# Kernel tuning notes

Measured on AMD Instinct MI355X. Metric: run time of the kernel, lower is better.

Reference implementation:

```python
import jax, jax.numpy as jnp
import numpy as np

N = 100000   # nodes
E = 1600000  # edges
G = 512      # graphs in batch
F_IN = 30
H = 128
EPS = 1e-5   # BatchNorm1d default eps


def setup_inputs() -> dict:
    key = jax.random.key(0)
    ks = jax.random.split(key, 16)
    x = jax.random.normal(ks[0], (N, F_IN), dtype=jnp.float32)
    edge_index = jax.random.randint(ks[1], (2, E), 0, N, dtype=jnp.int64)
    batch = jnp.sort(jax.random.randint(ks[2], (N,), 0, G, dtype=jnp.int64))
    d = {"x": x, "edge_index": edge_index, "batch": batch}
    dims = [(F_IN, H), (H, H), (H, H)]
    for i, (din, dout) in enumerate(dims):
        d[f"W{i}"] = jax.random.normal(ks[3 + i], (din, dout), dtype=jnp.float32) * (1.0 / np.sqrt(din))
        d[f"b{i}"] = jnp.zeros((dout,), dtype=jnp.float32)
        d[f"g{i}"] = jnp.ones((dout,), dtype=jnp.float32)   # BN gamma
        d[f"bt{i}"] = jnp.zeros((dout,), dtype=jnp.float32)  # BN beta
    d["HW1"] = jax.random.normal(ks[9], (H, 64), dtype=jnp.float32) * (1.0 / np.sqrt(H))
    d["Hb1"] = jnp.zeros((64,), dtype=jnp.float32)
    d["HW2"] = jax.random.normal(ks[10], (64, 1), dtype=jnp.float32) * 0.125
    d["Hb2"] = jnp.zeros((1,), dtype=jnp.float32)
    return d


def _bn(x, gamma, beta):
    # training-mode BatchNorm1d over node dim, biased variance (as torch uses for normalization)
    mu = jnp.mean(x, axis=0)
    var = jnp.mean(jnp.square(x - mu), axis=0)
    return (x - mu) * jax.lax.rsqrt(var + EPS) * gamma + beta


def reference(x, edge_index, batch, W0, b0, g0, bt0, W1, b1, g1, bt1, W2, b2, g2, bt2, HW1, Hb1, HW2, Hb2):
    # GCNConv: add self-loops, symmetric D^{-1/2}(A+I)D^{-1/2} normalization
    loop = jnp.arange(N, dtype=edge_index.dtype)
    src = jnp.concatenate([edge_index[0], loop])  # [E+N]
    dst = jnp.concatenate([edge_index[1], loop])
    deg = jax.ops.segment_sum(jnp.ones(src.shape, jnp.float32), dst, num_segments=N)
    dinv = jax.lax.rsqrt(jnp.maximum(deg, 1.0))  # deg >= 1 due to self-loops
    norm = (dinv[src] * dinv[dst])[:, None]      # [E+N, 1]

    for W, b, g, bt in ((W0, b0, g0, bt0), (W1, b1, g1, bt1), (W2, b2, g2, bt2)):
        h = x @ W                                           # [N, H]
        agg = jax.ops.segment_sum(h[src] * norm, dst, num_segments=N) + b
        x = jnp.maximum(_bn(agg, g, bt), 0.0)               # BN + ReLU (dropout = identity here)

    # global_mean_pool over graph ids
    counts = jax.ops.segment_sum(jnp.ones((N,), jnp.float32), batch, num_segments=G)
    pooled = jax.ops.segment_sum(x, batch, num_segments=G) / jnp.maximum(counts, 1.0)[:, None]

    h = jnp.maximum(pooled @ HW1 + Hb1, 0.0)
    return (h @ HW2 + Hb2).squeeze(-1)  # [G]
```

## Files before the change

### kernel.cpp

```cpp
#include <hip/hip_runtime.h>

#define BN_EPS 1e-5f
#define BSH 8

typedef __attribute__((ext_vector_type(8))) short bf16x8;
typedef __attribute__((ext_vector_type(4))) float f32x4;

__device__ inline float bfhi(unsigned int v) { return __uint_as_float(v & 0xFFFF0000u); }
__device__ inline float bflo(unsigned int v) { return __uint_as_float(v << 16); }
__device__ inline unsigned short f2bf(float f) {
  unsigned int u = __float_as_uint(f);
  u += 0x7FFFu + ((u >> 16) & 1u);
  return (unsigned short)(u >> 16);
}
__device__ inline unsigned int pack2bf(float lo, float hi) {
  return (unsigned int)f2bf(lo) | ((unsigned int)f2bf(hi) << 16);
}

__global__ void k_bucket(const int* __restrict__ src, const int* __restrict__ dst,
                         int* __restrict__ gcur, uint2* __restrict__ sedge,
                         int NB, int CAP, int E) {
  __shared__ int lh[512], rb[512];
  int tid = threadIdx.x;
  for (int i = tid; i < NB; i += 256) lh[i] = 0;
  __syncthreads();
  int base = blockIdx.x * 8192;
  int lim = min(8192, E - base);
  for (int i = tid; i < lim; i += 256)
    atomicAdd(&lh[dst[base + i] >> BSH], 1);
  __syncthreads();
  for (int i = tid; i < NB; i += 256) {
    int c = lh[i];
    rb[i] = c ? atomicAdd(&gcur[i], c) : 0;
    lh[i] = 0;
  }
  __syncthreads();
  for (int i = tid; i < lim; i += 256) {
    int d = dst[base + i];
    int s = src[base + i];
    int b = d >> BSH;
    int pos = rb[b] + atomicAdd(&lh[b], 1);
    if (pos < CAP) {
      uint2 v; v.x = (unsigned int)s; v.y = (unsigned int)d;
      sedge[(size_t)b * CAP + pos] = v;
    }
  }
}

__global__ void k_csr1(const uint2* __restrict__ sedge, const int* __restrict__ gcur,
                       int* __restrict__ startv, int* __restrict__ cnt,
                       float* __restrict__ dinv, int CAP, int n) {
  int b = blockIdx.x, tid = threadIdx.x;
  __shared__ int h[256], sc[256];
  h[tid] = 0;
  __syncthreads();
  int cb = gcur[b]; if (cb > CAP) cb = CAP;
  const uint2* sd = sedge + (size_t)b * CAP;
  for (int i = tid; i < cb; i += 256) atomicAdd(&h[sd[i].y & 255], 1);
  __syncthreads();
  int v = h[tid];
  sc[tid] = v;
  __syncthreads();
  for (int o = 1; o < 256; o <<= 1) {
    int t = (tid >= o) ? sc[tid - o] : 0;
    __syncthreads();
    sc[tid] += t;
    __syncthreads();
  }
  int gd = (b << BSH) + tid;
  if (gd < n) {
    startv[gd] = b * CAP + (sc[tid] - v);
    cnt[gd] = v;
    dinv[gd] = rsqrtf((float)v + 1.0f);
  }
}

__global__ void k_csr2(const uint2* __restrict__ sedge, const int* __restrict__ gcur,
                       const int* __restrict__ startv, const float* __restrict__ dinv,
                       unsigned int* __restrict__ elist, int CAP, int n) {
  int b = blockIdx.x, tid = threadIdx.x;
  __shared__ int cur[256];
  int gd = (b << BSH) + tid;
  cur[tid] = (gd < n) ? startv[gd] : 0;
  __syncthreads();
  int cb = gcur[b]; if (cb > CAP) cb = CAP;
  const uint2* sd = sedge + (size_t)b * CAP;
  for (int i = tid; i < cb; i += 256) {
    uint2 e = sd[i];
    int pos = atomicAdd(&cur[e.y & 255], 1);
    unsigned int u = (unsigned int)(dinv[e.x] * 32767.0f + 0.5f);
    elist[pos] = e.x | (u << 17);
  }
}

__global__ void k_cvtall(const float* __restrict__ x, const float* __restrict__ W0,
                         const float* __restrict__ W1, const float* __restrict__ W2,
                         unsigned short* __restrict__ xb, unsigned short* __restrict__ Wt0,
                         unsigned short* __restrict__ Wt1, unsigned short* __restrict__ Wt2,
                         int n) {
  int t = blockIdx.x * blockDim.x + threadIdx.x;
  if (t < 4096) {
    int nn = t >> 5, k = t & 31;
    Wt0[t] = f2bf(k < 30 ? W0[k * 128 + nn] : 0.f);
  } else if (t < 20480) {
    int i = t - 4096; int nn = i >> 7, k = i & 127;
    Wt1[i] = f2bf(W1[k * 128 + nn]);
  } else if (t < 36864) {
    int i = t - 20480; int nn = i >> 7, k = i & 127;
    Wt2[i] = f2bf(W2[k * 128 + nn]);
  } else {
    int i = t - 36864;
    if (i < n * 32) {
      int row = i >> 5, c = i & 31;
      xb[i] = f2bf(c < 30 ? x[row * 30 + c] : 0.f);
    }
  }
}

__global__ void k_gather0(const unsigned int* __restrict__ elist, const int* __restrict__ start,
                          const int* __restrict__ cnt, const float* __restrict__ dinv,
                          const uint4* __restrict__ x4,
                          unsigned int* __restrict__ G0, int n) {
  int lane = threadIdx.x & 63;
  int wv   = threadIdx.x >> 6;
  int grp  = lane >> 2;
  int q4   = lane & 3;
  int row  = blockIdx.x * 4 + wv;
  bool active = row < n;

  float acc[8];
  float di = 0.f, dq = 0.f;
  int len = 0;
  const unsigned int* ep = elist;
  if (active) {
    di = dinv[row];
    dq = di * (1.0f / 32767.0f);
    len = cnt[row];
    ep = elist + start[row];
  }
  {
    float selfw = (grp == 0 && active) ? di * di : 0.f;
    uint4 hv = (grp == 0 && active) ? x4[(size_t)row * 4 + q4] : make_uint4(0, 0, 0, 0);
    acc[0] = bflo(hv.x) * selfw; acc[1] = bfhi(hv.x) * selfw;
    acc[2] = bflo(hv.y) * selfw; acc[3] = bfhi(hv.y) * selfw;
    acc[4] = bflo(hv.z) * selfw; acc[5] = bfhi(hv.z) * selfw;
    acc[6] = bflo(hv.w) * selfw; acc[7] = bfhi(hv.w) * selfw;
  }
  for (int j = 0; j < len; j += 16) {
    int jj = j + grp;
    unsigned int e = (jj < len) ? ep[jj] : 0u;
    uint4 v = x4[(size_t)(e & 0x1FFFFu) * 4 + q4];
    float w = (float)(e >> 17) * dq;
    acc[0] = fmaf(bflo(v.x), w, acc[0]); acc[1] = fmaf(bfhi(v.x), w, acc[1]);
    acc[2] = fmaf(bflo(v.y), w, acc[2]); acc[3] = fmaf(bfhi(v.y), w, acc[3]);
    acc[4] = fmaf(bflo(v.z), w, acc[4]); acc[5] = fmaf(bfhi(v.z), w, acc[5]);
    acc[6] = fmaf(bflo(v.w), w, acc[6]); acc[7] = fmaf(bfhi(v.w), w, acc[7]);
  }
#pragma unroll
  for (int k = 0; k < 8; ++k) {
    acc[k] += __shfl_xor(acc[k], 4);
    acc[k] += __shfl_xor(acc[k], 8);
    acc[k] += __shfl_xor(acc[k], 16);
    acc[k] += __shfl_xor(acc[k], 32);
  }
  if (grp == 0 && active) {
    uint4 o;
    o.x = pack2bf(acc[0], acc[1]);
    o.y = pack2bf(acc[2], acc[3]);
    o.z = pack2bf(acc[4], acc[5]);
    o.w = pack2bf(acc[6], acc[7]);
    ((uint4*)G0)[(size_t)row * 4 + q4] = o;
  }
}

__global__ void k_gemm_mfma(const unsigned short* __restrict__ A,
                            const unsigned short* __restrict__ Wt,
                            const float* __restrict__ scsh, int doBN,
                            const float* __restrict__ bias, float* __restrict__ bnslab,
                            int doStats, unsigned short* __restrict__ C, int n, int Kp) {
  __shared__ float ssc[128], ssh[128];
  if (doBN) {
    if (threadIdx.x < 128) {
      ssc[threadIdx.x] = scsh[threadIdx.x];
      ssh[threadIdx.x] = scsh[128 + threadIdx.x];
    }
    __syncthreads();
  }
  int wave = threadIdx.x >> 6;
  int lane = threadIdx.x & 63;
  int m0 = blockIdx.x * 128 + wave * 32;
  int lm = lane & 15;
  int lq = lane >> 4;

  f32x4 acc[2][8] = {};
  const unsigned short* Arow0 = A + (size_t)(m0 + lm) * Kp + lq * 8;
  const unsigned short* Arow1 = Arow0 + (size_t)16 * Kp;
  const unsigned short* Bbase = Wt + (size_t)lm * Kp + lq * 8;

  for (int k0 = 0; k0 < Kp; k0 += 32) {
    uint4 ra0 = *(const uint4*)(Arow0 + k0);
    uint4 ra1 = *(const uint4*)(Arow1 + k0);
    bf16x8 a0, a1;
    if (doBN) {
      int cb = k0 + lq * 8;
      unsigned int w0 = pack2bf(fmaxf(fmaf(bflo(ra0.x), ssc[cb+0], ssh[cb+0]), 0.f),
                                fmaxf(fmaf(bfhi(ra0.x), ssc[cb+1], ssh[cb+1]), 0.f));
      unsigned int w1 = pack2bf(fmaxf(fmaf(bflo(ra0.y), ssc[cb+2], ssh[cb+2]), 0.f),
                                fmaxf(fmaf(bfhi(ra0.y), ssc[cb+3], ssh[cb+3]), 0.f));
      unsigned int w2 = pack2bf(fmaxf(fmaf(bflo(ra0.z), ssc[cb+4], ssh[cb+4]), 0.f),
                                fmaxf(fmaf(bfhi(ra0.z), ssc[cb+5], ssh[cb+5]), 0.f));
      unsigned int w3 = pack2bf(fmaxf(fmaf(bflo(ra0.w), ssc[cb+6], ssh[cb+6]), 0.f),
                                fmaxf(fmaf(bfhi(ra0.w), ssc[cb+7], ssh[cb+7]), 0.f));
      uint4 pa0 = make_uint4(w0, w1, w2, w3);
      a0 = *(bf16x8*)&pa0;
      unsigned int y0 = pack2bf(fmaxf(fmaf(bflo(ra1.x), ssc[cb+0], ssh[cb+0]), 0.f),
                                fmaxf(fmaf(bfhi(ra1.x), ssc[cb+1], ssh[cb+1]), 0.f));
      unsigned int y1 = pack2bf(fmaxf(fmaf(bflo(ra1.y), ssc[cb+2], ssh[cb+2]), 0.f),
                                fmaxf(fmaf(bfhi(ra1.y), ssc[cb+3], ssh[cb+3]), 0.f));
      unsigned int y2 = pack2bf(fmaxf(fmaf(bflo(ra1.z), ssc[cb+4], ssh[cb+4]), 0.f),
                                fmaxf(fmaf(bfhi(ra1.z), ssc[cb+5], ssh[cb+5]), 0.f));
      unsigned int y3 = pack2bf(fmaxf(fmaf(bflo(ra1.w), ssc[cb+6], ssh[cb+6]), 0.f),
                                fmaxf(fmaf(bfhi(ra1.w), ssc[cb+7], ssh[cb+7]), 0.f));
      uint4 pa1 = make_uint4(y0, y1, y2, y3);
      a1 = *(bf16x8*)&pa1;
    } else {
      a0 = *(bf16x8*)&ra0;
      a1 = *(bf16x8*)&ra1;
    }
#pragma unroll
    for (int t = 0; t < 8; ++t) {
      bf16x8 b = *(const bf16x8*)(Bbase + (size_t)t * 16 * Kp + k0);
      acc[0][t] = __builtin_amdgcn_mfma_f32_16x16x32_bf16(a0, b, acc[0][t], 0, 0, 0);
      acc[1][t] = __builtin_amdgcn_mfma_f32_16x16x32_bf16(a1, b, acc[1][t], 0, 0, 0);
    }
  }

#pragma unroll
  for (int h = 0; h < 2; ++h) {
    int rbase = m0 + h * 16 + lq * 4;
#pragma unroll
    for (int t = 0; t < 8; ++t) {
      int col = t * 16 + lm;
      float bv = doStats ? bias[col] : 0.f;
#pragma unroll
      for (int r = 0; r < 4; ++r) {
        int row = rbase + r;
        if (row < n) C[(size_t)row * 128 + col] = f2bf(acc[h][t][r] + bv);
      }
    }
  }

  if (doStats) {
    __shared__ float sms[4][256];
#pragma unroll
    for (int t = 0; t < 8; ++t) {
      int col = t * 16 + lm;
      float bv = bias[col];
      float s = 0.f, s2 = 0.f;
#pragma unroll
      for (int h = 0; h < 2; ++h) {
        int rbase = m0 + h * 16 + lq * 4;
#pragma unroll
        for (int r = 0; r < 4; ++r) {
          if (rbase + r < n) {
            float v = acc[h][t][r] + bv;
            s += v; s2 = fmaf(v, v, s2);
          }
        }
      }
      s  += __shfl_xor(s, 16);  s  += __shfl_xor(s, 32);
      s2 += __shfl_xor(s2, 16); s2 += __shfl_xor(s2, 32);
      if (lq == 0) { sms[wave][col] = s; sms[wave][128 + col] = s2; }
    }
    __syncthreads();
    int tid = threadIdx.x;
    int slab = (blockIdx.x & 63) * 256;
    float tot = sms[0][tid] + sms[1][tid] + sms[2][tid] + sms[3][tid];
    atomicAdd(&bnslab[slab + tid], tot);
  }
}

__global__ void k_gather(const unsigned int* __restrict__ elist, const int* __restrict__ start,
                         const int* __restrict__ cnt, const float* __restrict__ dinv,
                         const uint4* __restrict__ h4,
                         const float* __restrict__ bias, unsigned int* __restrict__ agg,
                         float* __restrict__ bnsumP, int n) {
  int lane = threadIdx.x & 63;
  int wv   = threadIdx.x >> 6;
  int grp  = lane >> 4;
  int c8   = lane & 15;
  int row  = blockIdx.x * 4 + wv;
  bool active = row < n;

  float acc[8];
  float di = 0.f, dq = 0.f;
  int len = 0;
  const unsigned int* ep = elist;

  if (active) {
    di = dinv[row];
    dq = di * (1.0f / 32767.0f);
    len = cnt[row];
    ep = elist + start[row];
  }

  {
    float selfw = (grp == 0 && active) ? di * di : 0.f;
    float4 b0 = make_float4(0.f, 0.f, 0.f, 0.f), b1 = b0;
    if (grp == 0 && active) {
      b0 = ((const float4*)bias)[c8 * 2];
      b1 = ((const float4*)bias)[c8 * 2 + 1];
    }
    uint4 hv = active ? h4[(size_t)row * 16 + c8] : make_uint4(0, 0, 0, 0);
    acc[0] = fmaf(bflo(hv.x), selfw, b0.x);
    acc[1] = fmaf(bfhi(hv.x), selfw, b0.y);
    acc[2] = fmaf(bflo(hv.y), selfw, b0.z);
    acc[3] = fmaf(bfhi(hv.y), selfw, b0.w);
    acc[4] = fmaf(bflo(hv.z), selfw, b1.x);
    acc[5] = fmaf(bfhi(hv.z), selfw, b1.y);
    acc[6] = fmaf(bflo(hv.w), selfw, b1.z);
    acc[7] = fmaf(bfhi(hv.w), selfw, b1.w);
  }

  int j = 0;
  for (; j + 8 <= len; j += 8) {
    unsigned int e0 = ep[j + grp];
    unsigned int e1 = ep[j + 4 + grp];
    uint4 v0 = h4[(size_t)(e0 & 0x1FFFFu) * 16 + c8];
    uint4 v1 = h4[(size_t)(e1 & 0x1FFFFu) * 16 + c8];
    float w0 = (float)(e0 >> 17) * dq;
    float w1 = (float)(e1 >> 17) * dq;
    acc[0] = fmaf(bflo(v0.x), w0, acc[0]); acc[1] = fmaf(bfhi(v0.x), w0, acc[1]);
    acc[2] = fmaf(bflo(v0.y), w0, acc[2]); acc[3] = fmaf(bfhi(v0.y), w0, acc[3]);
    acc[4] = fmaf(bflo(v0.z), w0, acc[4]); acc[5] = fmaf(bfhi(v0.z), w0, acc[5]);
    acc[6] = fmaf(bflo(v0.w), w0, acc[6]); acc[7] = fmaf(bfhi(v0.w), w0, acc[7]);
    acc[0] = fmaf(bflo(v1.x), w1, acc[0]); acc[1] = fmaf(bfhi(v1.x), w1, acc[1]);
    acc[2] = fmaf(bflo(v1.y), w1, acc[2]); acc[3] = fmaf(bfhi(v1.y), w1, acc[3]);
    acc[4] = fmaf(bflo(v1.z), w1, acc[4]); acc[5] = fmaf(bfhi(v1.z), w1, acc[5]);
    acc[6] = fmaf(bflo(v1.w), w1, acc[6]); acc[7] = fmaf(bfhi(v1.w), w1, acc[7]);
  }
  for (; j < len; j += 4) {
    int jj = j + grp;
    unsigned int e = (jj < len) ? ep[jj] : 0u;
    uint4 v = h4[(size_t)(e & 0x1FFFFu) * 16 + c8];
    float w = (float)(e >> 17) * dq;
    acc[0] = fmaf(bflo(v.x), w, acc[0]); acc[1] = fmaf(bfhi(v.x), w, acc[1]);
    acc[2] = fmaf(bflo(v.y), w, acc[2]); acc[3] = fmaf(bfhi(v.y), w, acc[3]);
    acc[4] = fmaf(bflo(v.z), w, acc[4]); acc[5] = fmaf(bfhi(v.z), w, acc[5]);
    acc[6] = fmaf(bflo(v.w), w, acc[6]); acc[7] = fmaf(bfhi(v.w), w, acc[7]);
  }

#pragma unroll
  for (int k = 0; k < 8; ++k) {
    acc[k] += __shfl_xor(acc[k], 16);
    acc[k] += __shfl_xor(acc[k], 32);
  }

  __shared__ float sm[2][4][128];
  if (lane < 16) {
    if (active) {
      uint4 o;
      o.x = pack2bf(acc[0], acc[1]);
      o.y = pack2bf(acc[2], acc[3]);
      o.z = pack2bf(acc[4], acc[5]);
      o.w = pack2bf(acc[6], acc[7]);
      ((uint4*)agg)[(size_t)row * 16 + c8] = o;
    }
#pragma unroll
    for (int k = 0; k < 8; ++k) {
      float a = acc[k];
      sm[0][wv][c8 * 8 + k] = a;
      sm[1][wv][c8 * 8 + k] = a * a;
    }
  }
  __syncthreads();
  int tid = threadIdx.x;
  int slab = (blockIdx.x & 63) * 256;
  if (tid < 128) {
    float s = sm[0][0][tid] + sm[0][1][tid] + sm[0][2][tid] + sm[0][3][tid];
    atomicAdd(&bnsumP[slab + tid], s);
  } else {
    int c = tid - 128;
    float s = sm[1][0][c] + sm[1][1][c] + sm[1][2][c] + sm[1][3][c];
    atomicAdd(&bnsumP[slab + 128 + c], s);
  }
}

__global__ void k_bnfinal(const float* __restrict__ bnsumP, const float* __restrict__ gamma,
                          const float* __restrict__ beta, float* __restrict__ scsh, int n) {
  int tid = threadIdx.x;
  int c = tid & 127;
  int which = tid >> 7;
  float s = 0.f;
  for (int k = 0; k < 64; ++k) s += bnsumP[k * 256 + which * 128 + c];
  __shared__ float sh[256];
  sh[tid] = s;
  __syncthreads();
  if (tid < 128) {
    float invn = 1.0f / (float)n;
    float mu  = sh[tid] * invn;
    float ex2 = sh[128 + tid] * invn;
    float var = fmaxf(ex2 - mu * mu, 0.f);
    float sc = gamma[tid] * rsqrtf(var + BN_EPS);
    scsh[tid] = sc;
    scsh[128 + tid] = fmaf(-mu, sc, beta[tid]);
  }
}

__global__ void k_poolhead(const unsigned int* __restrict__ aggd, const float* __restrict__ scsh,
                           const int* __restrict__ batch, const float* __restrict__ HW1,
                           const float* __restrict__ Hb1, const float* __restrict__ HW2,
                           const float* __restrict__ Hb2, float* __restrict__ out, int n) {
  int g = blockIdx.x;
  int wv = threadIdx.x >> 6, t = threadIdx.x & 63;
  int lo = 0, hi = n;
  while (lo < hi) { int mid = (lo + hi) >> 1; if (batch[mid] < g) lo = mid + 1; else hi = mid; }
  int s = lo;
  lo = 0; hi = n;
  int g1 = g + 1;
  while (lo < hi) { int mid = (lo + hi) >> 1; if (batch[mid] < g1) lo = mid + 1; else hi = mid; }
  int e = lo;

  float sc0 = scsh[2 * t], sc1 = scsh[2 * t + 1];
  float sh0 = scsh[128 + 2 * t], sh1 = scsh[128 + 2 * t + 1];
  float a0 = 0.f, a1 = 0.f;
  for (int i = s + wv; i < e; i += 4) {
    unsigned int u = aggd[(size_t)i * 64 + t];
    a0 += fmaxf(fmaf(bflo(u), sc0, sh0), 0.f);
    a1 += fmaxf(fmaf(bfhi(u), sc1, sh1), 0.f);
  }
  __shared__ float pp[4][128];
  pp[wv][2 * t] = a0;
  pp[wv][2 * t + 1] = a1;
  __syncthreads();
  if (wv == 0) {
    float inv = 1.0f / fmaxf((float)(e - s), 1.f);
    float p0 = (pp[0][2 * t] + pp[1][2 * t] + pp[2][2 * t] + pp[3][2 * t]) * inv;
    float p1 = (pp[0][2 * t + 1] + pp[1][2 * t + 1] + pp[2][2 * t + 1] + pp[3][2 * t + 1]) * inv;
    pp[0][2 * t] = p0;
    pp[0][2 * t + 1] = p1;
    float acc = Hb1[t];
    for (int k = 0; k < 128; ++k) acc = fmaf(pp[0][k], HW1[k * 64 + t], acc);
    float v = fmaxf(acc, 0.f) * HW2[t];
    for (int off = 32; off > 0; off >>= 1) v += __shfl_down(v, off);
    if (t == 0) out[g] = v + Hb2[0];
  }
}

extern "C" void kernel_launch(void* const* d_in, const int* in_sizes, int n_in,
                              void* d_out, int out_size, void* d_ws, size_t ws_size,
                              hipStream_t stream) {
  const int F_IN = 30, H = 128;
  const float* x   = (const float*)d_in[0];
  const int* eidx  = (const int*)d_in[1];
  const int* batch = (const int*)d_in[2];
  const int N = in_sizes[0] / F_IN;
  const int E = in_sizes[1] / 2;
  const int G = out_size;
  const int* srcp = eidx;
  const int* dstp = eidx + E;
  const float* HW1 = (const float*)d_in[15];
  const float* Hb1 = (const float*)d_in[16];
  const float* HW2 = (const float*)d_in[17];
  const float* Hb2 = (const float*)d_in[18];
  float* outp = (float*)d_out;

  const int Npad = (N + 127) & ~127;
  size_t nh = (size_t)Npad * H;
  const int NB = (N + 255) >> BSH;
  const int CAP = ((E / NB) * 3) / 2 + 128;
  const int NBpad = (NB + 63) & ~63;

  unsigned short* bufH = (unsigned short*)d_ws;
  unsigned short* bufX = bufH + nh;
  unsigned short* xbf  = bufX + nh;
  unsigned short* G0   = xbf + (size_t)Npad * 32;
  float* dinv = (float*)(G0 + (size_t)Npad * 32);
  int*   cnt    = (int*)(dinv + N);
  int*   startv = cnt + N;
  int*   gcur   = startv + N;
  float* bnsumP = (float*)(gcur + NBpad);
  float* scsh   = bnsumP + 3 * 64 * 256;
  unsigned short* Wt0 = (unsigned short*)(scsh + 256);
  unsigned short* Wt1 = Wt0 + 128 * 32;
  unsigned short* Wt2 = Wt1 + 128 * 128;
  unsigned int* elist = (unsigned int*)(Wt2 + 128 * 128 + 64);
  uint2* sedge = (uint2*)bufX;

  hipMemsetAsync(gcur, 0, ((size_t)NBpad + 3 * 64 * 256) * sizeof(int), stream);

  k_bucket<<<(E + 8191) / 8192, 256, 0, stream>>>(srcp, dstp, gcur, sedge, NB, CAP, E);
  k_csr1<<<NB, 256, 0, stream>>>(sedge, gcur, startv, cnt, dinv, CAP, N);
  k_csr2<<<NB, 256, 0, stream>>>(sedge, gcur, startv, dinv, elist, CAP, N);

  k_cvtall<<<(36864 + N * 32 + 255) / 256, 256, 0, stream>>>(
      x, (const float*)d_in[3], (const float*)d_in[7], (const float*)d_in[11],
      xbf, Wt0, Wt1, Wt2, N);

  const float* b0  = (const float*)d_in[4];
  const float* gm0 = (const float*)d_in[5];
  const float* bt0 = (const float*)d_in[6];

  k_gather0<<<(N + 3) / 4, 256, 0, stream>>>(elist, startv, cnt, dinv,
                                             (const uint4*)xbf, (unsigned int*)G0, N);
  k_gemm_mfma<<<Npad / 128, 256, 0, stream>>>(G0, Wt0, scsh, 0, b0, bnsumP, 1,
                                              bufX, N, 32);
  k_bnfinal<<<1, 256, 0, stream>>>(bnsumP, gm0, bt0, scsh, N);

  const unsigned short* Wts[3] = {nullptr, Wt1, Wt2};
  for (int l = 1; l < 3; ++l) {
    const float* b  = (const float*)d_in[4 + l * 4];
    const float* gm = (const float*)d_in[5 + l * 4];
    const float* bt = (const float*)d_in[6 + l * 4];
    float* bnslab = bnsumP + (size_t)l * 64 * 256;

    k_gemm_mfma<<<Npad / 128, 256, 0, stream>>>(bufX, Wts[l], scsh, 1, nullptr, nullptr, 0,
                                                bufH, N, 128);
    k_gather<<<(N + 3) / 4, 256, 0, stream>>>(elist, startv, cnt, dinv,
                                              (const uint4*)bufH, b,
                                              (unsigned int*)bufX, bnslab, N);
    k_bnfinal<<<1, 256, 0, stream>>>(bnslab, gm, bt, scsh, N);
  }

  k_poolhead<<<G, 256, 0, stream>>>((const unsigned int*)bufX, scsh, batch,
                                    HW1, Hb1, HW2, Hb2, outp, N);
}
```

Baseline: 455.3 us.

## Fuse BN finalize into producers, merge prep kernels, restructure gathers

Merges the edge bucketing and the bf16 conversion into one launch. It removes the three single-block BN finalize kernels by having the last-arriving block, detected through an atomic done counter, compute scale and shift. k_gather0 now processes 4 rows per wave with 4 edge slots each instead of 16 slots on one row. k_gather loops over 8 rows per wave, accumulates BN statistics in registers to cut shared-memory and atomic traffic, and uses nontemporal stores. The aim is fewer launches and less per-row reduction overhead, at the cost of a last-block serialization tail and reduced parallelism per launch.

```diff
diff --git a/kernel.cpp b/kernel.cpp
--- a/kernel.cpp
+++ b/kernel.cpp
@@ -5,6 +5,7 @@
 
 typedef __attribute__((ext_vector_type(8))) short bf16x8;
 typedef __attribute__((ext_vector_type(4))) float f32x4;
+typedef __attribute__((ext_vector_type(4))) unsigned int u32x4;
 
 __device__ inline float bfhi(unsigned int v) { return __uint_as_float(v & 0xFFFF0000u); }
 __device__ inline float bflo(unsigned int v) { return __uint_as_float(v << 16); }
@@ -17,32 +18,79 @@
   return (unsigned int)f2bf(lo) | ((unsigned int)f2bf(hi) << 16);
 }
 
-__global__ void k_bucket(const int* __restrict__ src, const int* __restrict__ dst,
-                         int* __restrict__ gcur, uint2* __restrict__ sedge,
-                         int NB, int CAP, int E) {
-  __shared__ int lh[512], rb[512];
-  int tid = threadIdx.x;
-  for (int i = tid; i < NB; i += 256) lh[i] = 0;
-  __syncthreads();
-  int base = blockIdx.x * 8192;
-  int lim = min(8192, E - base);
-  for (int i = tid; i < lim; i += 256)
-    atomicAdd(&lh[dst[base + i] >> BSH], 1);
-  __syncthreads();
-  for (int i = tid; i < NB; i += 256) {
-    int c = lh[i];
-    rb[i] = c ? atomicAdd(&gcur[i], c) : 0;
-    lh[i] = 0;
-  }
-  __syncthreads();
-  for (int i = tid; i < lim; i += 256) {
-    int d = dst[base + i];
-    int s = src[base + i];
-    int b = d >> BSH;
-    int pos = rb[b] + atomicAdd(&lh[b], 1);
-    if (pos < CAP) {
-      uint2 v; v.x = (unsigned int)s; v.y = (unsigned int)d;
-      sedge[(size_t)b * CAP + pos] = v;
+__device__ inline void bn_finalize(float* __restrict__ bnslab, const float* __restrict__ gamma,
+                                   const float* __restrict__ beta, float* __restrict__ scsh,
+                                   int n, int tid) {
+  if (tid < 128) {
+    float ss = 0.f, ss2 = 0.f;
+    for (int k = 0; k < 64; ++k) {
+      ss  += __hip_atomic_load(&bnslab[k * 256 + tid], __ATOMIC_RELAXED, __HIP_MEMORY_SCOPE_AGENT);
+      ss2 += __hip_atomic_load(&bnslab[k * 256 + 128 + tid], __ATOMIC_RELAXED, __HIP_MEMORY_SCOPE_AGENT);
+    }
+    float invn = 1.0f / (float)n;
+    float mu  = ss * invn;
+    float var = fmaxf(ss2 * invn - mu * mu, 0.f);
+    float sc = gamma[tid] * rsqrtf(var + BN_EPS);
+    scsh[tid] = sc;
+    scsh[128 + tid] = fmaf(-mu, sc, beta[tid]);
+  }
+}
+
+__global__ void k_prep(const int* __restrict__ src, const int* __restrict__ dst,
+                       int* __restrict__ gcur, uint2* __restrict__ sedge,
+                       int NB, int CAP, int E, int BB,
+                       const float* __restrict__ x, const float* __restrict__ W0,
+                       const float* __restrict__ W1, const float* __restrict__ W2,
+                       unsigned short* __restrict__ xb, unsigned short* __restrict__ Wt0,
+                       unsigned short* __restrict__ Wt1, unsigned short* __restrict__ Wt2,
+                       int n) {
+  if ((int)blockIdx.x < BB) {
+    __shared__ int lh[512], rb[512];
+    int tid = threadIdx.x;
+    for (int i = tid; i < NB; i += 256) lh[i] = 0;
+    __syncthreads();
+    int base = blockIdx.x * 8192;
+    int lim = min(8192, E - base);
+    for (int i = tid; i < lim; i += 256)
+      atomicAdd(&lh[dst[base + i] >> BSH], 1);
+    __syncthreads();
+    for (int i = tid; i < NB; i += 256) {
+      int c = lh[i];
+      rb[i] = c ? atomicAdd(&gcur[i], c) : 0;
+      lh[i] = 0;
+    }
+    __syncthreads();
+    for (int i = tid; i < lim; i += 256) {
+      int d = dst[base + i];
+      int s = src[base + i];
+      int b = d >> BSH;
+      int pos = rb[b] + atomicAdd(&lh[b], 1);
+      if (pos < CAP) {
+        uint2 v; v.x = (unsigned int)s; v.y = (unsigned int)d;
+        sedge[(size_t)b * CAP + pos] = v;
+      }
+    }
+  } else {
+    int t0 = (((int)blockIdx.x - BB) * 256 + (int)threadIdx.x) * 4;
+#pragma unroll
+    for (int u = 0; u < 4; ++u) {
+      int t = t0 + u;
+      if (t < 4096) {
+        int nn = t >> 5, k = t & 31;
+        Wt0[t] = f2bf(k < 30 ? W0[k * 128 + nn] : 0.f);
+      } else if (t < 20480) {
+        int i = t - 4096; int nn = i >> 7, k = i & 127;
+        Wt1[i] = f2bf(W1[k * 128 + nn]);
+      } else if (t < 36864) {
+        int i = t - 20480; int nn = i >> 7, k = i & 127;
+        Wt2[i] = f2bf(W2[k * 128 + nn]);
+      } else {
+        int i = t - 36864;
+        if (i < n * 32) {
+          int row = i >> 5, c = i & 31;
+          xb[i] = f2bf(c < 30 ? x[row * 30 + c] : 0.f);
+        }
+      }
     }
   }
 }
@@ -93,39 +141,16 @@
   }
 }
 
-__global__ void k_cvtall(const float* __restrict__ x, const float* __restrict__ W0,
-                         const float* __restrict__ W1, const float* __restrict__ W2,
-                         unsigned short* __restrict__ xb, unsigned short* __restrict__ Wt0,
-                         unsigned short* __restrict__ Wt1, unsigned short* __restrict__ Wt2,
-                         int n) {
-  int t = blockIdx.x * blockDim.x + threadIdx.x;
-  if (t < 4096) {
-    int nn = t >> 5, k = t & 31;
-    Wt0[t] = f2bf(k < 30 ? W0[k * 128 + nn] : 0.f);
-  } else if (t < 20480) {
-    int i = t - 4096; int nn = i >> 7, k = i & 127;
-    Wt1[i] = f2bf(W1[k * 128 + nn]);
-  } else if (t < 36864) {
-    int i = t - 20480; int nn = i >> 7, k = i & 127;
-    Wt2[i] = f2bf(W2[k * 128 + nn]);
-  } else {
-    int i = t - 36864;
-    if (i < n * 32) {
-      int row = i >> 5, c = i & 31;
-      xb[i] = f2bf(c < 30 ? x[row * 30 + c] : 0.f);
-    }
-  }
-}
-
 __global__ void k_gather0(const unsigned int* __restrict__ elist, const int* __restrict__ start,
                           const int* __restrict__ cnt, const float* __restrict__ dinv,
                           const uint4* __restrict__ x4,
                           unsigned int* __restrict__ G0, int n) {
   int lane = threadIdx.x & 63;
   int wv   = threadIdx.x >> 6;
-  int grp  = lane >> 2;
+  int r4   = lane >> 4;
+  int slot = (lane >> 2) & 3;
   int q4   = lane & 3;
-  int row  = blockIdx.x * 4 + wv;
+  int row  = blockIdx.x * 16 + wv * 4 + r4;
   bool active = row < n;
 
   float acc[8];
@@ -139,15 +164,15 @@
     ep = elist + start[row];
   }
   {
-    float selfw = (grp == 0 && active) ? di * di : 0.f;
-    uint4 hv = (grp == 0 && active) ? x4[(size_t)row * 4 + q4] : make_uint4(0, 0, 0, 0);
+    float selfw = (slot == 0 && active) ? di * di : 0.f;
+    uint4 hv = (slot == 0 && active) ? x4[(size_t)row * 4 + q4] : make_uint4(0, 0, 0, 0);
     acc[0] = bflo(hv.x) * selfw; acc[1] = bfhi(hv.x) * selfw;
     acc[2] = bflo(hv.y) * selfw; acc[3] = bfhi(hv.y) * selfw;
     acc[4] = bflo(hv.z) * selfw; acc[5] = bfhi(hv.z) * selfw;
     acc[6] = bflo(hv.w) * selfw; acc[7] = bfhi(hv.w) * selfw;
   }
-  for (int j = 0; j < len; j += 16) {
-    int jj = j + grp;
+  for (int j = 0; j < len; j += 4) {
+    int jj = j + slot;
     unsigned int e = (jj < len) ? ep[jj] : 0u;
     uint4 v = x4[(size_t)(e & 0x1FFFFu) * 4 + q4];
     float w = (float)(e >> 17) * dq;
@@ -160,10 +185,8 @@
   for (int k = 0; k < 8; ++k) {
     acc[k] += __shfl_xor(acc[k], 4);
     acc[k] += __shfl_xor(acc[k], 8);
-    acc[k] += __shfl_xor(acc[k], 16);
-    acc[k] += __shfl_xor(acc[k], 32);
-  }
-  if (grp == 0 && active) {
+  }
+  if (slot == 0 && active) {
     uint4 o;
     o.x = pack2bf(acc[0], acc[1]);
     o.y = pack2bf(acc[2], acc[3]);
@@ -177,7 +200,9 @@
                             const unsigned short* __restrict__ Wt,
                             const float* __restrict__ scsh, int doBN,
                             const float* __restrict__ bias, float* __restrict__ bnslab,
-                            int doStats, unsigned short* __restrict__ C, int n, int Kp) {
+                            int doStats, unsigned short* __restrict__ C, int n, int Kp,
+                            int* __restrict__ done, const float* __restrict__ gammaP,
+                            const float* __restrict__ betaP, float* __restrict__ scshOut) {
   __shared__ float ssc[128], ssh[128];
   if (doBN) {
     if (threadIdx.x < 128) {
@@ -277,6 +302,15 @@
     int slab = (blockIdx.x & 63) * 256;
     float tot = sms[0][tid] + sms[1][tid] + sms[2][tid] + sms[3][tid];
     atomicAdd(&bnslab[slab + tid], tot);
+    __syncthreads();
+    __shared__ int lastf;
+    if (tid == 0) {
+      __threadfence();
+      int old = __hip_atomic_fetch_add(done, 1, __ATOMIC_ACQ_REL, __HIP_MEMORY_SCOPE_AGENT);
+      lastf = (old == (int)gridDim.x - 1) ? 1 : 0;
+    }
+    __syncthreads();
+    if (lastf) bn_finalize(bnslab, gammaP, betaP, scshOut, n, tid);
   }
 }
 
@@ -284,127 +318,128 @@
                          const int* __restrict__ cnt, const float* __restrict__ dinv,
                          const uint4* __restrict__ h4,
                          const float* __restrict__ bias, unsigned int* __restrict__ agg,
-                         float* __restrict__ bnsumP, int n) {
+                         float* __restrict__ bnslab, int n, int* __restrict__ done,
+                         const float* __restrict__ gamma, const float* __restrict__ beta,
+                         float* __restrict__ scsh) {
   int lane = threadIdx.x & 63;
   int wv   = threadIdx.x >> 6;
   int grp  = lane >> 4;
   int c8   = lane & 15;
-  int row  = blockIdx.x * 4 + wv;
-  bool active = row < n;
-
-  float acc[8];
-  float di = 0.f, dq = 0.f;
-  int len = 0;
-  const unsigned int* ep = elist;
-
-  if (active) {
-    di = dinv[row];
-    dq = di * (1.0f / 32767.0f);
-    len = cnt[row];
-    ep = elist + start[row];
-  }
-
-  {
-    float selfw = (grp == 0 && active) ? di * di : 0.f;
-    float4 b0 = make_float4(0.f, 0.f, 0.f, 0.f), b1 = b0;
+  int rb   = blockIdx.x * 32 + wv * 8;
+
+  float sacc[8]  = {0.f, 0.f, 0.f, 0.f, 0.f, 0.f, 0.f, 0.f};
+  float s2acc[8] = {0.f, 0.f, 0.f, 0.f, 0.f, 0.f, 0.f, 0.f};
+
+  for (int r = 0; r < 8; ++r) {
+    int row = rb + r;
+    bool active = row < n;
+
+    float acc[8];
+    float di = 0.f, dq = 0.f;
+    int len = 0;
+    const unsigned int* ep = elist;
+    if (active) {
+      di = dinv[row];
+      dq = di * (1.0f / 32767.0f);
+      len = cnt[row];
+      ep = elist + start[row];
+    }
+    {
+      float selfw = (grp == 0 && active) ? di * di : 0.f;
+      float4 b0 = make_float4(0.f, 0.f, 0.f, 0.f), b1 = b0;
+      if (grp == 0 && active) {
+        b0 = ((const float4*)bias)[c8 * 2];
+        b1 = ((const float4*)bias)[c8 * 2 + 1];
+      }
+      uint4 hv = active ? h4[(size_t)row * 16 + c8] : make_uint4(0, 0, 0, 0);
+      acc[0] = fmaf(bflo(hv.x), selfw, b0.x);
+      acc[1] = fmaf(bfhi(hv.x), selfw, b0.y);
+      acc[2] = fmaf(bflo(hv.y), selfw, b0.z);
+      acc[3] = fmaf(bfhi(hv.y), selfw, b0.w);
+      acc[4] = fmaf(bflo(hv.z), selfw, b1.x);
+      acc[5] = fmaf(bfhi(hv.z), selfw, b1.y);
+      acc[6] = fmaf(bflo(hv.w), selfw, b1.z);
+      acc[7] = fmaf(bfhi(hv.w), selfw, b1.w);
+    }
+
+    int j = 0;
+    for (; j + 8 <= len; j += 8) {
+      unsigned int e0 = ep[j + grp];
+      unsigned int e1 = ep[j + 4 + grp];
+      uint4 v0 = h4[(size_t)(e0 & 0x1FFFFu) * 16 + c8];
+      uint4 v1 = h4[(size_t)(e1 & 0x1FFFFu) * 16 + c8];
+      float w0 = (float)(e0 >> 17) * dq;
+      float w1 = (float)(e1 >> 17) * dq;
+      acc[0] = fmaf(bflo(v0.x), w0, acc[0]); acc[1] = fmaf(bfhi(v0.x), w0, acc[1]);
+      acc[2] = fmaf(bflo(v0.y), w0, acc[2]); acc[3] = fmaf(bfhi(v0.y), w0, acc[3]);
+      acc[4] = fmaf(bflo(v0.z), w0, acc[4]); acc[5] = fmaf(bfhi(v0.z), w0, acc[5]);
+      acc[6] = fmaf(bflo(v0.w), w0, acc[6]); acc[7] = fmaf(bfhi(v0.w), w0, acc[7]);
+      acc[0] = fmaf(bflo(v1.x), w1, acc[0]); acc[1] = fmaf(bfhi(v1.x), w1, acc[1]);
+      acc[2] = fmaf(bflo(v1.y), w1, acc[2]); acc[3] = fmaf(bfhi(v1.y), w1, acc[3]);
+      acc[4] = fmaf(bflo(v1.z), w1, acc[4]); acc[5] = fmaf(bfhi(v1.z), w1, acc[5]);
+      acc[6] = fmaf(bflo(v1.w), w1, acc[6]); acc[7] = fmaf(bfhi(v1.w), w1, acc[7]);
+    }
+    for (; j < len; j += 4) {
+      int jj = j + grp;
+      unsigned int e = (jj < len) ? ep[jj] : 0u;
+      uint4 v = h4[(size_t)(e & 0x1FFFFu) * 16 + c8];
+      float w = (float)(e >> 17) * dq;
+      acc[0] = fmaf(bflo(v.x), w, acc[0]); acc[1] = fmaf(bfhi(v.x), w, acc[1]);
+      acc[2] = fmaf(bflo(v.y), w, acc[2]); acc[3] = fmaf(bfhi(v.y), w, acc[3]);
+      acc[4] = fmaf(bflo(v.z), w, acc[4]); acc[5] = fmaf(bfhi(v.z), w, acc[5]);
+      acc[6] = fmaf(bflo(v.w), w, acc[6]); acc[7] = fmaf(bfhi(v.w), w, acc[7]);
+    }
+
+#pragma unroll
+    for (int k = 0; k < 8; ++k) {
+      acc[k] += __shfl_xor(acc[k], 16);
+      acc[k] += __shfl_xor(acc[k], 32);
+    }
+
     if (grp == 0 && active) {
-      b0 = ((const float4*)bias)[c8 * 2];
-      b1 = ((const float4*)bias)[c8 * 2 + 1];
-    }
-    uint4 hv = active ? h4[(size_t)row * 16 + c8] : make_uint4(0, 0, 0, 0);
-    acc[0] = fmaf(bflo(hv.x), selfw, b0.x);
-    acc[1] = fmaf(bfhi(hv.x), selfw, b0.y);
-    acc[2] = fmaf(bflo(hv.y), selfw, b0.z);
-    acc[3] = fmaf(bfhi(hv.y), selfw, b0.w);
-    acc[4] = fmaf(bflo(hv.z), selfw, b1.x);
-    acc[5] = fmaf(bfhi(hv.z), selfw, b1.y);
-    acc[6] = fmaf(bflo(hv.w), selfw, b1.z);
-    acc[7] = fmaf(bfhi(hv.w), selfw, b1.w);
-  }
-
-  int j = 0;
-  for (; j + 8 <= len; j += 8) {
-    unsigned int e0 = ep[j + grp];
-    unsigned int e1 = ep[j + 4 + grp];
-    uint4 v0 = h4[(size_t)(e0 & 0x1FFFFu) * 16 + c8];
-    uint4 v1 = h4[(size_t)(e1 & 0x1FFFFu) * 16 + c8];
-    float w0 = (float)(e0 >> 17) * dq;
-    float w1 = (float)(e1 >> 17) * dq;
-    acc[0] = fmaf(bflo(v0.x), w0, acc[0]); acc[1] = fmaf(bfhi(v0.x), w0, acc[1]);
-    acc[2] = fmaf(bflo(v0.y), w0, acc[2]); acc[3] = fmaf(bfhi(v0.y), w0, acc[3]);
-    acc[4] = fmaf(bflo(v0.z), w0, acc[4]); acc[5] = fmaf(bfhi(v0.z), w0, acc[5]);
-    acc[6] = fmaf(bflo(v0.w), w0, acc[6]); acc[7] = fmaf(bfhi(v0.w), w0, acc[7]);
-    acc[0] = fmaf(bflo(v1.x), w1, acc[0]); acc[1] = fmaf(bfhi(v1.x), w1, acc[1]);
-    acc[2] = fmaf(bflo(v1.y), w1, acc[2]); acc[3] = fmaf(bfhi(v1.y), w1, acc[3]);
-    acc[4] = fmaf(bflo(v1.z), w1, acc[4]); acc[5] = fmaf(bfhi(v1.z), w1, acc[5]);
-    acc[6] = fmaf(bflo(v1.w), w1, acc[6]); acc[7] = fmaf(bfhi(v1.w), w1, acc[7]);
-  }
-  for (; j < len; j += 4) {
-    int jj = j + grp;
-    unsigned int e = (jj < len) ? ep[jj] : 0u;
-    uint4 v = h4[(size_t)(e & 0x1FFFFu) * 16 + c8];
-    float w = (float)(e >> 17) * dq;
-    acc[0] = fmaf(bflo(v.x), w, acc[0]); acc[1] = fmaf(bfhi(v.x), w, acc[1]);
-    acc[2] = fmaf(bflo(v.y), w, acc[2]); acc[3] = fmaf(bfhi(v.y), w, acc[3]);
-    acc[4] = fmaf(bflo(v.z), w, acc[4]); acc[5] = fmaf(bfhi(v.z), w, acc[5]);
-    acc[6] = fmaf(bflo(v.w), w, acc[6]); acc[7] = fmaf(bfhi(v.w), w, acc[7]);
-  }
-
-#pragma unroll
-  for (int k = 0; k < 8; ++k) {
-    acc[k] += __shfl_xor(acc[k], 16);
-    acc[k] += __shfl_xor(acc[k], 32);
-  }
-
-  __shared__ float sm[2][4][128];
-  if (lane < 16) {
-    if (active) {
-      uint4 o;
+      u32x4 o;
       o.x = pack2bf(acc[0], acc[1]);
       o.y = pack2bf(acc[2], acc[3]);
       o.z = pack2bf(acc[4], acc[5]);
       o.w = pack2bf(acc[6], acc[7]);
-      ((uint4*)agg)[(size_t)row * 16 + c8] = o;
+      __builtin_nontemporal_store(o, (u32x4*)agg + (size_t)row * 16 + c8);
     }
 #pragma unroll
     for (int k = 0; k < 8; ++k) {
-      float a = acc[k];
-      sm[0][wv][c8 * 8 + k] = a;
-      sm[1][wv][c8 * 8 + k] = a * a;
+      sacc[k] += acc[k];
+      s2acc[k] = fmaf(acc[k], acc[k], s2acc[k]);
+    }
+  }
+
+  __shared__ float sm[2][4][128];
+  if (lane < 16) {
+#pragma unroll
+    for (int k = 0; k < 8; ++k) {
+      sm[0][wv][c8 * 8 + k] = sacc[k];
+      sm[1][wv][c8 * 8 + k] = s2acc[k];
     }
   }
   __syncthreads();
   int tid = threadIdx.x;
   int slab = (blockIdx.x & 63) * 256;
+  float s;
   if (tid < 128) {
-    float s = sm[0][0][tid] + sm[0][1][tid] + sm[0][2][tid] + sm[0][3][tid];
-    atomicAdd(&bnsumP[slab + tid], s);
+    s = sm[0][0][tid] + sm[0][1][tid] + sm[0][2][tid] + sm[0][3][tid];
   } else {
     int c = tid - 128;
-    float s = sm[1][0][c] + sm[1][1][c] + sm[1][2][c] + sm[1][3][c];
-    atomicAdd(&bnsumP[slab + 128 + c], s);
-  }
-}
-
-__global__ void k_bnfinal(const float* __restrict__ bnsumP, const float* __restrict__ gamma,
-                          const float* __restrict__ beta, float* __restrict__ scsh, int n) {
-  int tid = threadIdx.x;
-  int c = tid & 127;
-  int which = tid >> 7;
-  float s = 0.f;
-  for (int k = 0; k < 64; ++k) s += bnsumP[k * 256 + which * 128 + c];
-  __shared__ float sh[256];
-  sh[tid] = s;
-  __syncthreads();
-  if (tid < 128) {
-    float invn = 1.0f / (float)n;
-    float mu  = sh[tid] * invn;
-    float ex2 = sh[128 + tid] * invn;
-    float var = fmaxf(ex2 - mu * mu, 0.f);
-    float sc = gamma[tid] * rsqrtf(var + BN_EPS);
-    scsh[tid] = sc;
-    scsh[128 + tid] = fmaf(-mu, sc, beta[tid]);
-  }
+    s = sm[1][0][c] + sm[1][1][c] + sm[1][2][c] + sm[1][3][c];
+  }
+  atomicAdd(&bnslab[slab + tid], s);
+
+  __syncthreads();
+  __shared__ int lastf;
+  if (tid == 0) {
+    __threadfence();
+    int old = __hip_atomic_fetch_add(done, 1, __ATOMIC_ACQ_REL, __HIP_MEMORY_SCOPE_AGENT);
+    lastf = (old == (int)gridDim.x - 1) ? 1 : 0;
+  }
+  __syncthreads();
+  if (lastf) bn_finalize(bnslab, gamma, beta, scsh, n, tid);
 }
 
 __global__ void k_poolhead(const unsigned int* __restrict__ aggd, const float* __restrict__ scsh,
@@ -480,32 +515,33 @@
   int*   startv = cnt + N;
   int*   gcur   = startv + N;
   float* bnsumP = (float*)(gcur + NBpad);
-  float* scsh   = bnsumP + 3 * 64 * 256;
+  int*   done   = (int*)(bnsumP + 3 * 64 * 256);
+  float* scsh   = (float*)(done + 4);
   unsigned short* Wt0 = (unsigned short*)(scsh + 256);
   unsigned short* Wt1 = Wt0 + 128 * 32;
   unsigned short* Wt2 = Wt1 + 128 * 128;
   unsigned int* elist = (unsigned int*)(Wt2 + 128 * 128 + 64);
   uint2* sedge = (uint2*)bufX;
 
-  hipMemsetAsync(gcur, 0, ((size_t)NBpad + 3 * 64 * 256) * sizeof(int), stream);
-
-  k_bucket<<<(E + 8191) / 8192, 256, 0, stream>>>(srcp, dstp, gcur, sedge, NB, CAP, E);
+  hipMemsetAsync(gcur, 0, ((size_t)NBpad + 3 * 64 * 256 + 4) * sizeof(int), stream);
+
+  const int BB = (E + 8191) / 8192;
+  const int TT = 36864 + N * 32;
+  const int CV = (TT + 1023) >> 10;
+  k_prep<<<BB + CV, 256, 0, stream>>>(srcp, dstp, gcur, sedge, NB, CAP, E, BB,
+                                      x, (const float*)d_in[3], (const float*)d_in[7],
+                                      (const float*)d_in[11], xbf, Wt0, Wt1, Wt2, N);
   k_csr1<<<NB, 256, 0, stream>>>(sedge, gcur, startv, cnt, dinv, CAP, N);
   k_csr2<<<NB, 256, 0, stream>>>(sedge, gcur, startv, dinv, elist, CAP, N);
-
-  k_cvtall<<<(36864 + N * 32 + 255) / 256, 256, 0, stream>>>(
-      x, (const float*)d_in[3], (const float*)d_in[7], (const float*)d_in[11],
-      xbf, Wt0, Wt1, Wt2, N);
 
   const float* b0  = (const float*)d_in[4];
   const float* gm0 = (const float*)d_in[5];
   const float* bt0 = (const float*)d_in[6];
 
-  k_gather0<<<(N + 3) / 4, 256, 0, stream>>>(elist, startv, cnt, dinv,
-                                             (const uint4*)xbf, (unsigned int*)G0, N);
+  k_gather0<<<(N + 15) / 16, 256, 0, stream>>>(elist, startv, cnt, dinv,
+                                               (const uint4*)xbf, (unsigned int*)G0, N);
   k_gemm_mfma<<<Npad / 128, 256, 0, stream>>>(G0, Wt0, scsh, 0, b0, bnsumP, 1,
-                                              bufX, N, 32);
-  k_bnfinal<<<1, 256, 0, stream>>>(bnsumP, gm0, bt0, scsh, N);
+                                              bufX, N, 32, done + 0, gm0, bt0, scsh);
 
   const unsigned short* Wts[3] = {nullptr, Wt1, Wt2};
   for (int l = 1; l < 3; ++l) {
@@ -515,11 +551,11 @@
     float* bnslab = bnsumP + (size_t)l * 64 * 256;
 
     k_gemm_mfma<<<Npad / 128, 256, 0, stream>>>(bufX, Wts[l], scsh, 1, nullptr, nullptr, 0,
-                                                bufH, N, 128);
-    k_gather<<<(N + 3) / 4, 256, 0, stream>>>(elist, startv, cnt, dinv,
-                                              (const uint4*)bufH, b,
-                                              (unsigned int*)bufX, bnslab, N);
-    k_bnfinal<<<1, 256, 0, stream>>>(bnslab, gm, bt, scsh, N);
+                                                bufH, N, 128, nullptr, nullptr, nullptr, nullptr);
+    k_gather<<<(N + 31) / 32, 256, 0, stream>>>(elist, startv, cnt, dinv,
+                                                (const uint4*)bufH, b,
+                                                (unsigned int*)bufX, bnslab, N,
+                                                done + l, gm, bt, scsh);
   }
 
   k_poolhead<<<G, 256, 0, stream>>>((const unsigned int*)bufX, scsh, batch,
```

Measured after the change: 784.2 us. 1.72x slower.

## Fold BN finalize into consumers and merge bucket/convert prep kernels

Applied to the files above, without the earlier changes.

Removes the three single-block BN finalize kernels: each consuming GEMM block and the pool/head kernel now reduces the 64 partial stat slabs itself and computes scale/shift in shared memory. The edge bucketing and the bf16 conversion of x and the weights are merged into one launch, with extra blocks doing conversion (4 elements per thread). This cuts five kernel launches and their serialization gaps, in exchange for redundant per-block reduction work (64 loads per thread in every GEMM block) and a heterogeneous combined kernel.

```diff
diff --git a/kernel.cpp b/kernel.cpp
--- a/kernel.cpp
+++ b/kernel.cpp
@@ -17,32 +17,61 @@
   return (unsigned int)f2bf(lo) | ((unsigned int)f2bf(hi) << 16);
 }
 
-__global__ void k_bucket(const int* __restrict__ src, const int* __restrict__ dst,
-                         int* __restrict__ gcur, uint2* __restrict__ sedge,
-                         int NB, int CAP, int E) {
-  __shared__ int lh[512], rb[512];
-  int tid = threadIdx.x;
-  for (int i = tid; i < NB; i += 256) lh[i] = 0;
-  __syncthreads();
-  int base = blockIdx.x * 8192;
-  int lim = min(8192, E - base);
-  for (int i = tid; i < lim; i += 256)
-    atomicAdd(&lh[dst[base + i] >> BSH], 1);
-  __syncthreads();
-  for (int i = tid; i < NB; i += 256) {
-    int c = lh[i];
-    rb[i] = c ? atomicAdd(&gcur[i], c) : 0;
-    lh[i] = 0;
-  }
-  __syncthreads();
-  for (int i = tid; i < lim; i += 256) {
-    int d = dst[base + i];
-    int s = src[base + i];
-    int b = d >> BSH;
-    int pos = rb[b] + atomicAdd(&lh[b], 1);
-    if (pos < CAP) {
-      uint2 v; v.x = (unsigned int)s; v.y = (unsigned int)d;
-      sedge[(size_t)b * CAP + pos] = v;
+__global__ void k_prep(const int* __restrict__ src, const int* __restrict__ dst,
+                       int* __restrict__ gcur, uint2* __restrict__ sedge,
+                       int NB, int CAP, int E, int BB,
+                       const float* __restrict__ x, const float* __restrict__ W0,
+                       const float* __restrict__ W1, const float* __restrict__ W2,
+                       unsigned short* __restrict__ xb, unsigned short* __restrict__ Wt0,
+                       unsigned short* __restrict__ Wt1, unsigned short* __restrict__ Wt2,
+                       int n) {
+  if ((int)blockIdx.x < BB) {
+    __shared__ int lh[512], rb[512];
+    int tid = threadIdx.x;
+    for (int i = tid; i < NB; i += 256) lh[i] = 0;
+    __syncthreads();
+    int base = blockIdx.x * 8192;
+    int lim = min(8192, E - base);
+    for (int i = tid; i < lim; i += 256)
+      atomicAdd(&lh[dst[base + i] >> BSH], 1);
+    __syncthreads();
+    for (int i = tid; i < NB; i += 256) {
+      int c = lh[i];
+      rb[i] = c ? atomicAdd(&gcur[i], c) : 0;
+      lh[i] = 0;
+    }
+    __syncthreads();
+    for (int i = tid; i < lim; i += 256) {
+      int d = dst[base + i];
+      int s = src[base + i];
+      int b = d >> BSH;
+      int pos = rb[b] + atomicAdd(&lh[b], 1);
+      if (pos < CAP) {
+        uint2 v; v.x = (unsigned int)s; v.y = (unsigned int)d;
+        sedge[(size_t)b * CAP + pos] = v;
+      }
+    }
+  } else {
+    int t0 = (((int)blockIdx.x - BB) * 256 + (int)threadIdx.x) * 4;
+#pragma unroll
+    for (int u = 0; u < 4; ++u) {
+      int t = t0 + u;
+      if (t < 4096) {
+        int nn = t >> 5, k = t & 31;
+        Wt0[t] = f2bf(k < 30 ? W0[k * 128 + nn] : 0.f);
+      } else if (t < 20480) {
+        int i = t - 4096; int nn = i >> 7, k = i & 127;
+        Wt1[i] = f2bf(W1[k * 128 + nn]);
+      } else if (t < 36864) {
+        int i = t - 20480; int nn = i >> 7, k = i & 127;
+        Wt2[i] = f2bf(W2[k * 128 + nn]);
+      } else {
+        int i = t - 36864;
+        if (i < n * 32) {
+          int row = i >> 5, c = i & 31;
+          xb[i] = f2bf(c < 30 ? x[row * 30 + c] : 0.f);
+        }
+      }
     }
   }
 }
@@ -93,30 +122,6 @@
   }
 }
 
-__global__ void k_cvtall(const float* __restrict__ x, const float* __restrict__ W0,
-                         const float* __restrict__ W1, const float* __restrict__ W2,
-                         unsigned short* __restrict__ xb, unsigned short* __restrict__ Wt0,
-                         unsigned short* __restrict__ Wt1, unsigned short* __restrict__ Wt2,
-                         int n) {
-  int t = blockIdx.x * blockDim.x + threadIdx.x;
-  if (t < 4096) {
-    int nn = t >> 5, k = t & 31;
-    Wt0[t] = f2bf(k < 30 ? W0[k * 128 + nn] : 0.f);
-  } else if (t < 20480) {
-    int i = t - 4096; int nn = i >> 7, k = i & 127;
-    Wt1[i] = f2bf(W1[k * 128 + nn]);
-  } else if (t < 36864) {
-    int i = t - 20480; int nn = i >> 7, k = i & 127;
-    Wt2[i] = f2bf(W2[k * 128 + nn]);
-  } else {
-    int i = t - 36864;
-    if (i < n * 32) {
-      int row = i >> 5, c = i & 31;
-      xb[i] = f2bf(c < 30 ? x[row * 30 + c] : 0.f);
-    }
-  }
-}
-
 __global__ void k_gather0(const unsigned int* __restrict__ elist, const int* __restrict__ start,
                           const int* __restrict__ cnt, const float* __restrict__ dinv,
                           const uint4* __restrict__ x4,
@@ -175,14 +180,26 @@
 
 __global__ void k_gemm_mfma(const unsigned short* __restrict__ A,
                             const unsigned short* __restrict__ Wt,
-                            const float* __restrict__ scsh, int doBN,
+                            const float* __restrict__ bnIn, const float* __restrict__ gamma,
+                            const float* __restrict__ beta, int doBN,
                             const float* __restrict__ bias, float* __restrict__ bnslab,
                             int doStats, unsigned short* __restrict__ C, int n, int Kp) {
   __shared__ float ssc[128], ssh[128];
   if (doBN) {
-    if (threadIdx.x < 128) {
-      ssc[threadIdx.x] = scsh[threadIdx.x];
-      ssh[threadIdx.x] = scsh[128 + threadIdx.x];
+    __shared__ float red[256];
+    int tid = threadIdx.x;
+    int which = tid >> 7, c = tid & 127;
+    float s = 0.f;
+    for (int k = 0; k < 64; ++k) s += bnIn[k * 256 + which * 128 + c];
+    red[tid] = s;
+    __syncthreads();
+    if (tid < 128) {
+      float invn = 1.0f / (float)n;
+      float mu  = red[tid] * invn;
+      float var = fmaxf(red[128 + tid] * invn - mu * mu, 0.f);
+      float sc  = gamma[tid] * rsqrtf(var + BN_EPS);
+      ssc[tid] = sc;
+      ssh[tid] = fmaf(-mu, sc, beta[tid]);
     }
     __syncthreads();
   }
@@ -386,31 +403,30 @@
   }
 }
 
-__global__ void k_bnfinal(const float* __restrict__ bnsumP, const float* __restrict__ gamma,
-                          const float* __restrict__ beta, float* __restrict__ scsh, int n) {
-  int tid = threadIdx.x;
-  int c = tid & 127;
-  int which = tid >> 7;
-  float s = 0.f;
-  for (int k = 0; k < 64; ++k) s += bnsumP[k * 256 + which * 128 + c];
-  __shared__ float sh[256];
-  sh[tid] = s;
-  __syncthreads();
-  if (tid < 128) {
-    float invn = 1.0f / (float)n;
-    float mu  = sh[tid] * invn;
-    float ex2 = sh[128 + tid] * invn;
-    float var = fmaxf(ex2 - mu * mu, 0.f);
-    float sc = gamma[tid] * rsqrtf(var + BN_EPS);
-    scsh[tid] = sc;
-    scsh[128 + tid] = fmaf(-mu, sc, beta[tid]);
-  }
-}
-
-__global__ void k_poolhead(const unsigned int* __restrict__ aggd, const float* __restrict__ scsh,
+__global__ void k_poolhead(const unsigned int* __restrict__ aggd, const float* __restrict__ bnIn,
+                           const float* __restrict__ gamma, const float* __restrict__ beta,
                            const int* __restrict__ batch, const float* __restrict__ HW1,
                            const float* __restrict__ Hb1, const float* __restrict__ HW2,
                            const float* __restrict__ Hb2, float* __restrict__ out, int n) {
+  __shared__ float bsc[128], bsh[128];
+  {
+    __shared__ float red[256];
+    int tid = threadIdx.x;
+    int which = tid >> 7, c = tid & 127;
+    float s = 0.f;
+    for (int k = 0; k < 64; ++k) s += bnIn[k * 256 + which * 128 + c];
+    red[tid] = s;
+    __syncthreads();
+    if (tid < 128) {
+      float invn = 1.0f / (float)n;
+      float mu  = red[tid] * invn;
+      float var = fmaxf(red[128 + tid] * invn - mu * mu, 0.f);
+      float sc  = gamma[tid] * rsqrtf(var + BN_EPS);
+      bsc[tid] = sc;
+      bsh[tid] = fmaf(-mu, sc, beta[tid]);
+    }
+    __syncthreads();
+  }
   int g = blockIdx.x;
   int wv = threadIdx.x >> 6, t = threadIdx.x & 63;
   int lo = 0, hi = n;
@@ -421,8 +437,8 @@
   while (lo < hi) { int mid = (lo + hi) >> 1; if (batch[mid] < g1) lo = mid + 1; else hi = mid; }
   int e = lo;
 
-  float sc0 = scsh[2 * t], sc1 = scsh[2 * t + 1];
-  float sh0 = scsh[128 + 2 * t], sh1 = scsh[128 + 2 * t + 1];
+  float sc0 = bsc[2 * t], sc1 = bsc[2 * t + 1];
+  float sh0 = bsh[2 * t], sh1 = bsh[2 * t + 1];
   float a0 = 0.f, a1 = 0.f;
   for (int i = s + wv; i < e; i += 4) {
     unsigned int u = aggd[(size_t)i * 64 + t];
@@ -480,8 +496,7 @@
   int*   startv = cnt + N;
   int*   gcur   = startv + N;
   float* bnsumP = (float*)(gcur + NBpad);
-  float* scsh   = bnsumP + 3 * 64 * 256;
-  unsigned short* Wt0 = (unsigned short*)(scsh + 256);
+  unsigned short* Wt0 = (unsigned short*)(bnsumP + 3 * 64 * 256);
   unsigned short* Wt1 = Wt0 + 128 * 32;
   unsigned short* Wt2 = Wt1 + 128 * 128;
   unsigned int* elist = (unsigned int*)(Wt2 + 128 * 128 + 64);
@@ -489,39 +504,46 @@
 
   hipMemsetAsync(gcur, 0, ((size_t)NBpad + 3 * 64 * 256) * sizeof(int), stream);
 
-  k_bucket<<<(E + 8191) / 8192, 256, 0, stream>>>(srcp, dstp, gcur, sedge, NB, CAP, E);
+  const int BB = (E + 8191) / 8192;
+  const int TT = 36864 + N * 32;
+  const int CV = (TT + 1023) >> 10;
+  k_prep<<<BB + CV, 256, 0, stream>>>(srcp, dstp, gcur, sedge, NB, CAP, E, BB,
+                                      x, (const float*)d_in[3], (const float*)d_in[7],
+                                      (const float*)d_in[11], xbf, Wt0, Wt1, Wt2, N);
   k_csr1<<<NB, 256, 0, stream>>>(sedge, gcur, startv, cnt, dinv, CAP, N);
   k_csr2<<<NB, 256, 0, stream>>>(sedge, gcur, startv, dinv, elist, CAP, N);
-
-  k_cvtall<<<(36864 + N * 32 + 255) / 256, 256, 0, stream>>>(
-      x, (const float*)d_in[3], (const float*)d_in[7], (const float*)d_in[11],
-      xbf, Wt0, Wt1, Wt2, N);
 
   const float* b0  = (const float*)d_in[4];
   const float* gm0 = (const float*)d_in[5];
   const float* bt0 = (const float*)d_in[6];
+  const float* b1  = (const float*)d_in[8];
+  const float* gm1 = (const float*)d_in[9];
+  const float* bt1 = (const float*)d_in[10];
+  const float* b2  = (const float*)d_in[12];
+  const float* gm2 = (const float*)d_in[13];
+  const float* bt2 = (const float*)d_in[14];
+
+  float* slab0 = bnsumP;
+  float* slab1 = bnsumP + (size_t)1 * 64 * 256;
+  float* slab2 = bnsumP + (size_t)2 * 64 * 256;
 
   k_gather0<<<(N + 3) / 4, 256, 0, stream>>>(elist, startv, cnt, dinv,
                                              (const uint4*)xbf, (unsigned int*)G0, N);
-  k_gemm_mfma<<<Npad / 128, 256, 0, stream>>>(G0, Wt0, scsh, 0, b0, bnsumP, 1,
-                                              bufX, N, 32);
-  k_bnfinal<<<1, 256, 0, stream>>>(bnsumP, gm0, bt0, scsh, N);
-
-  const unsigned short* Wts[3] = {nullptr, Wt1, Wt2};
-  for (int l = 1; l < 3; ++l) {
-    const float* b  = (const float*)d_in[4 + l * 4];
-    const float* gm = (const float*)d_in[5 + l * 4];
-    const float* bt = (const float*)d_in[6 + l * 4];
-    float* bnslab = bnsumP + (size_t)l * 64 * 256;
-
-    k_gemm_mfma<<<Npad / 128, 256, 0, stream>>>(bufX, Wts[l], scsh, 1, nullptr, nullptr, 0,
-                                                bufH, N, 128);
-    k_gather<<<(N + 3) / 4, 256, 0, stream>>>(elist, startv, cnt, dinv,
-                                              (const uint4*)bufH, b,
-                                              (unsigned int*)bufX, bnslab, N);
-    k_bnfinal<<<1, 256, 0, stream>>>(bnslab, gm, bt, scsh, N);
-  }
-
-  k_poolhead<<<G, 256, 0, stream>>>((const unsigned int*)bufX, scsh, batch,
+  k_gemm_mfma<<<Npad / 128, 256, 0, stream>>>(G0, Wt0, nullptr, nullptr, nullptr, 0,
+                                              b0, slab0, 1, bufX, N, 32);
+
+  k_gemm_mfma<<<Npad / 128, 256, 0, stream>>>(bufX, Wt1, slab0, gm0, bt0, 1,
+                                              nullptr, nullptr, 0, bufH, N, 128);
+  k_gather<<<(N + 3) / 4, 256, 0, stream>>>(elist, startv, cnt, dinv,
+                                            (const uint4*)bufH, b1,
+                                            (unsigned int*)bufX, slab1, N);
+
+  k_gemm_mfma<<<Npad / 128, 256, 0, stream>>>(bufX, Wt2, slab1, gm1, bt1, 1,
+                                              nullptr, nullptr, 0, bufH, N, 128);
+  k_gather<<<(N + 3) / 4, 256, 0, stream>>>(elist, startv, cnt, dinv,
+                                            (const uint4*)bufH, b2,
+                                            (unsigned int*)bufX, slab2, N);
+
+  k_poolhead<<<G, 256, 0, stream>>>((const unsigned int*)bufX, slab2, gm2, bt2, batch,
                                     HW1, Hb1, HW2, Hb2, outp, N);
 }
```

Result: no change. 448.4 us (-1.5%).
